# Optimization experiments

Measured on AMD Instinct MI355X. Metric: run time of the kernel, lower is better.

## Reference

```python
import jax, jax.numpy as jnp
import numpy as np

# Config (matches init_kwargs)
B, DIM = 16, 768
HEADS, DHEAD = 12, 64
H_MEM, W_MEM = 16, 16           # memory grid; N = 256 tokens
MAX_AH, MAX_AW = 3, 3
N = H_MEM * W_MEM


def _area_pool(t):
    """t: [B', N, D] laid out on an H_MEM x W_MEM grid.
    Returns (area_sums [B', M, D], area_sizes [M]) over all rectangle sizes
    (ah, aw) with 1<=ah<=MAX_AH, 1<=aw<=MAX_AW, at every valid position,
    via a 2D integral image (summed-area table)."""
    Bp, _, D = t.shape
    g = t.reshape(Bp, H_MEM, W_MEM, D)
    I = jnp.cumsum(jnp.cumsum(g, axis=1), axis=2)
    I = jnp.pad(I, ((0, 0), (1, 0), (1, 0), (0, 0)))  # [B', H+1, W+1, D]
    sums, sizes = [], []
    for ah in range(1, MAX_AH + 1):
        for aw in range(1, MAX_AW + 1):
            s = (I[:, ah:, aw:] - I[:, :-ah, aw:]
                 - I[:, ah:, :-aw] + I[:, :-ah, :-aw])  # [B', H-ah+1, W-aw+1, D]
            n_pos = s.shape[1] * s.shape[2]
            sums.append(s.reshape(Bp, n_pos, D))
            sizes.append(np.full((n_pos,), float(ah * aw), dtype=np.float32))
    return jnp.concatenate(sums, axis=1), jnp.asarray(np.concatenate(sizes))


def setup_inputs() -> dict:
    key = jax.random.key(0)
    ks = jax.random.split(key, 10)
    s = 0.02
    d = dict(
        x=jax.random.normal(ks[0], (B, N, DIM), jnp.float32),
        # to_qkv: Linear(dim, 3*dim, bias=False); stored as (in, out)
        w_qkv=jax.random.normal(ks[1], (DIM, 3 * DIM), jnp.float32) * s,
        # per-head q/k/v projections (dim -> heads*dim_head) with bias
        w_q=jax.random.normal(ks[2], (DIM, HEADS * DHEAD), jnp.float32) * s,
        b_q=jnp.zeros((HEADS * DHEAD,), jnp.float32),
        w_k=jax.random.normal(ks[3], (DIM, HEADS * DHEAD), jnp.float32) * s,
        b_k=jnp.zeros((HEADS * DHEAD,), jnp.float32),
        w_v=jax.random.normal(ks[4], (DIM, HEADS * DHEAD), jnp.float32) * s,
        b_v=jnp.zeros((HEADS * DHEAD,), jnp.float32),
        # output projection (heads*dim_head -> dim)
        w_o=jax.random.normal(ks[5], (HEADS * DHEAD, DIM), jnp.float32) * s,
        b_o=jnp.zeros((DIM,), jnp.float32),
    )
    return d


def reference(x, w_qkv, w_q, b_q, w_k, b_k, w_v, b_v, w_o, b_o):
    # QKV projection + split: 'b n (qkv d) -> qkv b n d'
    qkv = x @ w_qkv                               # [B, N, 3*DIM]
    q, k, v = jnp.split(qkv, 3, axis=-1)          # each [B, N, DIM]

    def to_heads(t, w, b):                        # 'b n (h d) -> (b h) n d'
        return ((t @ w + b)
                .reshape(B, N, HEADS, DHEAD)
                .transpose(0, 2, 1, 3)
                .reshape(B * HEADS, N, DHEAD))

    qh = to_heads(q, w_q, b_q)
    kh = to_heads(k, w_k, b_k)
    vh = to_heads(v, w_v, b_v)

    # Area keys: mean over each area; area values: sum over each area.
    k_sum, sizes = _area_pool(kh)                 # [BH, M, d], [M]
    k_area = k_sum / sizes[None, :, None]
    v_area, _ = _area_pool(vh)                    # [BH, M, d]

    logits = jnp.einsum('bqd,bmd->bqm', qh, k_area)   # [BH, N, M]
    weights = jax.nn.softmax(logits, axis=-1)
    out = jnp.einsum('bqm,bmd->bqd', weights, v_area)  # [BH, N, d]

    # '(b h) n d -> b n (h d)' then output projection
    out = (out.reshape(B, HEADS, N, DHEAD)
              .transpose(0, 2, 1, 3)
              .reshape(B, N, HEADS * DHEAD))
    return out @ w_o + b_o
```

## Files before the change

kernel.cpp:

```cpp
#include <hip/hip_runtime.h>
#include <hip/hip_bf16.h>

typedef __hip_bfloat16 bf16;
typedef __attribute__((ext_vector_type(8))) short short8b;
typedef __attribute__((ext_vector_type(4))) short short4b;
typedef __attribute__((ext_vector_type(4))) float f32x4;

#define NAREA 2025
#define NAREA_PAD 2048

static __device__ __forceinline__ float b2f(bf16 x) { return __bfloat162float(x); }
static __device__ __forceinline__ short f2bs(float f) {
  bf16 h = __float2bfloat16(f);
  return *(short*)&h;
}

static __device__ __forceinline__ void gll16(const void* g, void* l) {
  __builtin_amdgcn_global_load_lds(
      (const __attribute__((address_space(1))) unsigned int*)(unsigned long long)g,
      (__attribute__((address_space(3))) unsigned int*)(unsigned int)(unsigned long long)l,
      16, 0, 0);
}

__global__ __launch_bounds__(256) void k_prep(
    const float* __restrict__ x, const float* __restrict__ wqkv,
    const float* __restrict__ wq, const float* __restrict__ wk,
    const float* __restrict__ wv,
    bf16* __restrict__ xb, bf16* __restrict__ wqkvb,
    bf16* __restrict__ wqT, bf16* __restrict__ wkT, bf16* __restrict__ wvT,
    int4* __restrict__ rectG, float* __restrict__ invG)
{
  __shared__ float tile[32][33];
  int b = blockIdx.x;
  if (b < 4800) {
    int idx = (b * 256 + threadIdx.x) * 4;
    const int NX = 4096 * 768;
    float4 v;
    bf16* d;
    if (idx < NX) { v = *(const float4*)(x + idx); d = xb + idx; }
    else { v = *(const float4*)(wqkv + (idx - NX)); d = wqkvb + (idx - NX); }
    short4b s = {f2bs(v.x), f2bs(v.y), f2bs(v.z), f2bs(v.w)};
    *(short4b*)d = s;
    return;
  }
  if (b < 6528) {
    int r = b - 4800;
    int z = r / 576; r -= z * 576;
    int by = r / 24, bx = r - by * 24;
    const float* src = (z == 0) ? wq : (z == 1) ? wk : wv;
    bf16* dst = (z == 0) ? wqT : (z == 1) ? wkT : wvT;
    int r0 = by * 32, c0 = bx * 32;
    int lx = threadIdx.x & 31, ly = threadIdx.x >> 5;
#pragma unroll
    for (int yy = 0; yy < 4; ++yy)
      tile[ly + yy * 8][lx] = src[(size_t)(r0 + ly + yy * 8) * 768 + c0 + lx];
    __syncthreads();
#pragma unroll
    for (int yy = 0; yy < 4; ++yy)
      dst[(size_t)(c0 + ly + yy * 8) * 768 + r0 + lx] =
          __float2bfloat16(tile[lx][ly + yy * 8]);
    return;
  }
  int m = (b - 6528) * 256 + threadIdx.x;
  if (m >= NAREA_PAD) return;
  int4 rc = make_int4(0, 0, 0, 0);
  float iv = 0.f;
  if (m < NAREA) {
    int rem = m, ah = 1, aw = 1, found = 0;
    for (int a = 1; a <= 3 && !found; ++a)
      for (int w = 1; w <= 3 && !found; ++w) {
        int np = (17 - a) * (17 - w);
        if (rem < np) { ah = a; aw = w; found = 1; }
        else rem -= np;
      }
    int cw = 17 - aw;
    int y = rem / cw, xx = rem - y * cw;
    rc.x = (y * 17 + xx) * 64;
    rc.y = (y * 17 + (xx + aw)) * 64;
    rc.z = ((y + ah) * 17 + xx) * 64;
    rc.w = ((y + ah) * 17 + (xx + aw)) * 64;
    iv = 1.0f / (float)(ah * aw);
  }
  rectG[m] = rc;
  invG[m] = iv;
}

__global__ __launch_bounds__(256) void k_tcast1(
    const float* __restrict__ src, bf16* __restrict__ dst)
{
  __shared__ float tile[32][33];
  int r0 = blockIdx.y * 32, c0 = blockIdx.x * 32;
  int lx = threadIdx.x & 31, ly = threadIdx.x >> 5;
#pragma unroll
  for (int yy = 0; yy < 4; ++yy)
    tile[ly + yy * 8][lx] = src[(size_t)(r0 + ly + yy * 8) * 768 + c0 + lx];
  __syncthreads();
#pragma unroll
  for (int yy = 0; yy < 4; ++yy)
    dst[(size_t)(c0 + ly + yy * 8) * 768 + r0 + lx] =
        __float2bfloat16(tile[lx][ly + yy * 8]);
}


__global__ __launch_bounds__(256) void k_combine_m(
    const bf16* __restrict__ wqkvb, const bf16* __restrict__ wqT,
    const bf16* __restrict__ wkT, const bf16* __restrict__ wvT,
    bf16* __restrict__ WcTb)
{
  __shared__ __align__(16) short As[2][128 * 32];
  __shared__ __align__(16) short Bs[2][128 * 32];
  const int t3 = blockIdx.z;
  const bf16* BT = (t3 == 0) ? wqT : (t3 == 1) ? wkT : wvT;
  const int m0 = blockIdx.y * 128, n0 = blockIdx.x * 128;
  const int tid = threadIdx.x, lane = tid & 63, w = tid >> 6;
  const int tt = lane & 15, q4 = lane >> 4;
  const int moff = (w & 1) * 64, noff = (w >> 1) * 64;
  const int r_a = tid >> 2, kc = (tid & 3) * 8;

  f32x4 acc[4][4];
#pragma unroll
  for (int i = 0; i < 4; ++i)
#pragma unroll
    for (int j = 0; j < 4; ++j) acc[i][j] = (f32x4){0.f, 0.f, 0.f, 0.f};

#define STAGE_C(k0, buf)                                                        \
  {                                                                             \
    gll16(wqkvb + (size_t)(m0 + r_a) * 2304 + t3 * 768 + (k0) + kc,             \
          &As[buf][w * 512]);                                                   \
    gll16(wqkvb + (size_t)(m0 + r_a + 64) * 2304 + t3 * 768 + (k0) + kc,        \
          &As[buf][2048 + w * 512]);                                            \
    gll16(BT + (size_t)(n0 + r_a) * 768 + (k0) + kc, &Bs[buf][w * 512]);        \
    gll16(BT + (size_t)(n0 + r_a + 64) * 768 + (k0) + kc,                       \
          &Bs[buf][2048 + w * 512]);                                            \
  }

  STAGE_C(0, 0);
  for (int it = 0; it < 24; ++it) {
    __syncthreads();
    if (it < 23) STAGE_C((it + 1) * 32, (it + 1) & 1);
    const short* as = As[it & 1];
    const short* bs = Bs[it & 1];
    short8b afr[4], bfr[4];
#pragma unroll
    for (int mt = 0; mt < 4; ++mt)
      afr[mt] = *(const short8b*)&as[(moff + mt * 16 + tt) * 32 + q4 * 8];
#pragma unroll
    for (int nt = 0; nt < 4; ++nt)
      bfr[nt] = *(const short8b*)&bs[(noff + nt * 16 + tt) * 32 + q4 * 8];
#pragma unroll
    for (int mt = 0; mt < 4; ++mt)
#pragma unroll
      for (int nt = 0; nt < 4; ++nt)
        acc[mt][nt] = __builtin_amdgcn_mfma_f32_16x16x32_bf16(afr[mt], bfr[nt], acc[mt][nt], 0, 0, 0);
  }
#undef STAGE_C

  bf16* C = WcTb + (size_t)t3 * 768 * 768;
#pragma unroll
  for (int nt = 0; nt < 4; ++nt) {
    int n = n0 + noff + nt * 16 + tt;
#pragma unroll
    for (int mt = 0; mt < 4; ++mt) {
      int mb = m0 + moff + mt * 16 + q4 * 4;
      short4b v = {f2bs(acc[mt][nt][0]), f2bs(acc[mt][nt][1]),
                   f2bs(acc[mt][nt][2]), f2bs(acc[mt][nt][3])};
      *(short4b*)&C[(size_t)n * 768 + mb] = v;
    }
  }
}

__global__ __launch_bounds__(256) void k_proj_m(
    const bf16* __restrict__ xb, const bf16* __restrict__ WcTb,
    const float* __restrict__ bq, const float* __restrict__ bk,
    const float* __restrict__ bv,
    bf16* __restrict__ qh, bf16* __restrict__ kh, bf16* __restrict__ vh)
{
  __shared__ __align__(16) short As[2][128 * 32];
  __shared__ __align__(16) short Bs[2][128 * 32];
  const int t3 = blockIdx.z;
  const bf16* BT = WcTb + (size_t)t3 * 768 * 768;
  const float* bias = (t3 == 0) ? bq : (t3 == 1) ? bk : bv;
  bf16* dst = (t3 == 0) ? qh : (t3 == 1) ? kh : vh;
  const int m0 = blockIdx.y * 128, n0 = blockIdx.x * 128;
  const int tid = threadIdx.x, lane = tid & 63, w = tid >> 6;
  const int tt = lane & 15, q4 = lane >> 4;
  const int moff = (w & 1) * 64, noff = (w >> 1) * 64;
  const int r_a = tid >> 2, kc = (tid & 3) * 8;

  f32x4 acc[4][4];
#pragma unroll
  for (int i = 0; i < 4; ++i)
#pragma unroll
    for (int j = 0; j < 4; ++j) acc[i][j] = (f32x4){0.f, 0.f, 0.f, 0.f};

#define STAGE_P(k0, buf)                                                        \
  {                                                                             \
    gll16(xb + (size_t)(m0 + r_a) * 768 + (k0) + kc, &As[buf][w * 512]);        \
    gll16(xb + (size_t)(m0 + r_a + 64) * 768 + (k0) + kc,                       \
          &As[buf][2048 + w * 512]);                                            \
    gll16(BT + (size_t)(n0 + r_a) * 768 + (k0) + kc, &Bs[buf][w * 512]);        \
    gll16(BT + (size_t)(n0 + r_a + 64) * 768 + (k0) + kc,                       \
          &Bs[buf][2048 + w * 512]);                                            \
  }

  STAGE_P(0, 0);
  for (int it = 0; it < 24; ++it) {
    __syncthreads();
    if (it < 23) STAGE_P((it + 1) * 32, (it + 1) & 1);
    const short* as = As[it & 1];
    const short* bs = Bs[it & 1];
    short8b afr[4], bfr[4];
#pragma unroll
    for (int mt = 0; mt < 4; ++mt)
      afr[mt] = *(const short8b*)&as[(moff + mt * 16 + tt) * 32 + q4 * 8];
#pragma unroll
    for (int nt = 0; nt < 4; ++nt)
      bfr[nt] = *(const short8b*)&bs[(noff + nt * 16 + tt) * 32 + q4 * 8];
#pragma unroll
    for (int mt = 0; mt < 4; ++mt)
#pragma unroll
      for (int nt = 0; nt < 4; ++nt)
        acc[mt][nt] = __builtin_amdgcn_mfma_f32_16x16x32_bf16(afr[mt], bfr[nt], acc[mt][nt], 0, 0, 0);
  }
#undef STAGE_P

#pragma unroll
  for (int nt = 0; nt < 4; ++nt) {
    int c = n0 + noff + nt * 16 + tt;
    float bvv = bias[c];
    int h = c >> 6, d = c & 63;
#pragma unroll
    for (int mt = 0; mt < 4; ++mt) {
#pragma unroll
      for (int r = 0; r < 4; ++r) {
        int m = m0 + moff + mt * 16 + q4 * 4 + r;
        dst[(((size_t)((m >> 8) * 12 + h)) << 14) + ((m & 255) << 6) + d] =
            __float2bfloat16(acc[mt][nt][r] + bvv);
      }
    }
  }
}

__global__ __launch_bounds__(256) void k_out_m(
    const bf16* __restrict__ attno, const bf16* __restrict__ woT,
    const float* __restrict__ bo, float* __restrict__ out)
{
  __shared__ __align__(16) short As[2][128 * 32];
  __shared__ __align__(16) short Bs[2][128 * 32];
  const int m0 = blockIdx.y * 128, n0 = blockIdx.x * 128;
  const int tid = threadIdx.x, lane = tid & 63, w = tid >> 6;
  const int tt = lane & 15, q4 = lane >> 4;
  const int moff = (w & 1) * 64, noff = (w >> 1) * 64;
  const int r_a = tid >> 2, kc = (tid & 3) * 8;
  const int m_a0 = m0 + r_a, m_a1 = m0 + r_a + 64;

  f32x4 acc[4][4];
#pragma unroll
  for (int i = 0; i < 4; ++i)
#pragma unroll
    for (int j = 0; j < 4; ++j) acc[i][j] = (f32x4){0.f, 0.f, 0.f, 0.f};

#define STAGE_O(k0, buf)                                                        \
  {                                                                             \
    int k = (k0) + kc;                                                          \
    gll16(attno + (((size_t)((m_a0 >> 8) * 12 + (k >> 6))) << 14) +             \
              ((m_a0 & 255) << 6) + (k & 63),                                   \
          &As[buf][w * 512]);                                                   \
    gll16(attno + (((size_t)((m_a1 >> 8) * 12 + (k >> 6))) << 14) +             \
              ((m_a1 & 255) << 6) + (k & 63),                                   \
          &As[buf][2048 + w * 512]);                                            \
    gll16(woT + (size_t)(n0 + r_a) * 768 + k, &Bs[buf][w * 512]);               \
    gll16(woT + (size_t)(n0 + r_a + 64) * 768 + k, &Bs[buf][2048 + w * 512]);   \
  }

  STAGE_O(0, 0);
  for (int it = 0; it < 24; ++it) {
    __syncthreads();
    if (it < 23) STAGE_O((it + 1) * 32, (it + 1) & 1);
    const short* as = As[it & 1];
    const short* bs = Bs[it & 1];
    short8b afr[4], bfr[4];
#pragma unroll
    for (int mt = 0; mt < 4; ++mt)
      afr[mt] = *(const short8b*)&as[(moff + mt * 16 + tt) * 32 + q4 * 8];
#pragma unroll
    for (int nt = 0; nt < 4; ++nt)
      bfr[nt] = *(const short8b*)&bs[(noff + nt * 16 + tt) * 32 + q4 * 8];
#pragma unroll
    for (int mt = 0; mt < 4; ++mt)
#pragma unroll
      for (int nt = 0; nt < 4; ++nt)
        acc[mt][nt] = __builtin_amdgcn_mfma_f32_16x16x32_bf16(afr[mt], bfr[nt], acc[mt][nt], 0, 0, 0);
  }
#undef STAGE_O

#pragma unroll
  for (int nt = 0; nt < 4; ++nt) {
    int c = n0 + noff + nt * 16 + tt;
    float bvv = bo[c];
#pragma unroll
    for (int mt = 0; mt < 4; ++mt)
#pragma unroll
      for (int r = 0; r < 4; ++r) {
        int m = m0 + moff + mt * 16 + q4 * 4 + r;
        out[(size_t)m * 768 + c] = acc[mt][nt][r] + bvv;
      }
  }
}

__global__ __launch_bounds__(1024) void k_area_pre(
    const bf16* __restrict__ kh, const bf16* __restrict__ vh,
    const int4* __restrict__ rectG, const float* __restrict__ invG,
    bf16* __restrict__ Karea, bf16* __restrict__ VareaT)
{
  __shared__ float sat[17 * 17 * 65];
  int bh = blockIdx.x >> 1;
  bool isv = blockIdx.x & 1;
  const bf16* src = (isv ? vh : kh) + ((size_t)bh << 14);
  int tid = threadIdx.x;
  int d = tid & 63;
  int row = tid >> 6;
  {
    float run = 0.f;
    sat[((row + 1) * 17) * 65 + d] = 0.f;
#pragma unroll
    for (int xx = 0; xx < 16; ++xx) {
      run += b2f(src[(row * 16 + xx) * 64 + d]);
      sat[((row + 1) * 17 + (xx + 1)) * 65 + d] = run;
    }
    if (row == 0) {
#pragma unroll
      for (int xx = 0; xx < 17; ++xx) sat[xx * 65 + d] = 0.f;
    }
  }
  __syncthreads();
  {
    int x = row + 1;
    float run = 0.f;
#pragma unroll
    for (int y = 1; y <= 16; ++y) {
      run += sat[(y * 17 + x) * 65 + d];
      sat[(y * 17 + x) * 65 + d] = run;
    }
  }
  __syncthreads();
  if (!isv) {
    bf16* out = Karea + ((size_t)bh << 17);
    for (int c = row; c < 45; c += 16) {
      int ah, y;
      if (c < 16)      { ah = 1; y = c; }
      else if (c < 31) { ah = 2; y = c - 16; }
      else             { ah = 3; y = c - 31; }
      int b1, b2, b3;
      if (ah == 1)      { b1 = 0;    b2 = 256;  b3 = 496;  }
      else if (ah == 2) { b1 = 720;  b2 = 960;  b3 = 1185; }
      else              { b1 = 1395; b2 = 1619; b3 = 1829; }
      float V[17];
#pragma unroll
      for (int x = 0; x < 17; ++x)
        V[x] = sat[((y + ah) * 17 + x) * 65 + d] - sat[(y * 17 + x) * 65 + d];
      {
        int b = b1 + y * 16;
#pragma unroll
        for (int x = 0; x < 16; ++x)
          out[(size_t)(b + x) * 64 + d] = __float2bfloat16((V[x + 1] - V[x]) * (1.0f / (float)(ah)));
      }
      {
        int b = b2 + y * 15;
        float iv = 1.0f / (float)(2 * ah);
#pragma unroll
        for (int x = 0; x < 15; ++x)
          out[(size_t)(b + x) * 64 + d] = __float2bfloat16((V[x + 2] - V[x]) * iv);
      }
      {
        int b = b3 + y * 14;
        float iv = 1.0f / (float)(3 * ah);
#pragma unroll
        for (int x = 0; x < 14; ++x)
          out[(size_t)(b + x) * 64 + d] = __float2bfloat16((V[x + 3] - V[x]) * iv);
      }
    }
    if (row == 15) {
      for (int m = NAREA; m < NAREA_PAD; ++m)
        out[(size_t)m * 64 + d] = __float2bfloat16(0.f);
    }
  } else {
    int mcol = tid & 63;
    int r16 = tid >> 6;
    bf16* out = VareaT + ((size_t)bh << 17);
    for (int s = 0; s < 128; ++s) {
      int idx = s * 16 + r16;
      int it = idx >> 6, dd = idx & 63;
      int4 rc = rectG[it * 64 + mcol];
      int cx = rc.x + (rc.x >> 6), cy = rc.y + (rc.y >> 6);
      int cz = rc.z + (rc.z >> 6), cw = rc.w + (rc.w >> 6);
      float df = sat[cw + dd] - sat[cy + dd] - sat[cz + dd] + sat[cx + dd];
      out[(((size_t)it << 6) + dd) * 64 + mcol] = __float2bfloat16(df);
    }
  }
}

__global__ __launch_bounds__(256, 4) void k_attn_g(
    const bf16* __restrict__ qh, const bf16* __restrict__ Karea,
    const bf16* __restrict__ VareaT,
    float* __restrict__ Op0, float* __restrict__ Op1,
    float* __restrict__ lp0, float* __restrict__ lp1)
{
  __shared__ __align__(16) short aK2[2][64 * 80];
  __shared__ __align__(16) short aVt2[2][64 * 80];

  const int tid = threadIdx.x;
  const int w = tid >> 6;
  const int lane = tid & 63;
  const int t = lane & 15;
  const int q4 = lane >> 4;
  const int bh = blockIdx.x;
  const int Q0 = blockIdx.y * 128;
  const int it0 = blockIdx.z * 16;
  const int rbase = (t & 12) * 2 + (t & 3);

  const bf16* Kb = Karea + ((size_t)bh << 17);
  const bf16* Vb = VareaT + ((size_t)bh << 17);
  const bf16* qrowA = qh + ((size_t)bh << 14) + (size_t)(Q0 + w * 32 + t) * 64;
  const bf16* qrowB = qrowA + 16 * 64;

  short8b qfA0 = *(const short8b*)(qrowA + q4 * 8);
  short8b qfA1 = *(const short8b*)(qrowA + 32 + q4 * 8);
  short8b qfB0 = *(const short8b*)(qrowB + q4 * 8);
  short8b qfB1 = *(const short8b*)(qrowB + 32 + q4 * 8);

  f32x4 OA[4], OB[4];
#pragma unroll
  for (int i = 0; i < 4; ++i) {
    OA[i] = (f32x4){0.f, 0.f, 0.f, 0.f};
    OB[i] = (f32x4){0.f, 0.f, 0.f, 0.f};
  }
  float lA = 0.f, lB = 0.f;

  const int a8 = tid >> 2;
  const int c8 = (tid & 3) * 16;

  {
    size_t off = ((size_t)(it0 * 64 + a8) << 6) + c8;
    short8b k0a = *(const short8b*)&Kb[off];
    short8b k0b = *(const short8b*)&Kb[off + 8];
    short8b v0a = *(const short8b*)&Vb[off];
    short8b v0b = *(const short8b*)&Vb[off + 8];
    *(short8b*)&aK2[0][a8 * 80 + c8] = k0a;
    *(short8b*)&aK2[0][a8 * 80 + c8 + 8] = k0b;
    *(short8b*)&aVt2[0][a8 * 80 + c8] = v0a;
    *(short8b*)&aVt2[0][a8 * 80 + c8 + 8] = v0b;
  }

  for (int it = it0; it < it0 + 16; ++it) {
    short8b kna, knb, vna, vnb;
    if (it + 1 < it0 + 16) {
      size_t off = ((size_t)((it + 1) * 64 + a8) << 6) + c8;
      kna = *(const short8b*)&Kb[off];
      knb = *(const short8b*)&Kb[off + 8];
      vna = *(const short8b*)&Vb[off];
      vnb = *(const short8b*)&Vb[off + 8];
    }
    __syncthreads();
    const short* aK = aK2[it & 1];
    const short* aVt = aVt2[it & 1];
    if (it + 1 < it0 + 16) {
      short* aKn = aK2[(it + 1) & 1];
      short* aVtn = aVt2[(it + 1) & 1];
      *(short8b*)&aKn[a8 * 80 + c8] = kna;
      *(short8b*)&aKn[a8 * 80 + c8 + 8] = knb;
      *(short8b*)&aVtn[a8 * 80 + c8] = vna;
      *(short8b*)&aVtn[a8 * 80 + c8 + 8] = vnb;
    }

    const int t0 = it * 64;
    const bool edge = (t0 + 64 > NAREA);
    union { short8b v; unsigned u[4]; } apvA[2], apvB[2];
#pragma unroll
    for (int at = 0; at < 4; ++at) {
      int row = rbase + (at & 1) * 4 + (at >> 1) * 32;
      short8b af0 = *(const short8b*)&aK[row * 80 + q4 * 8];
      short8b af1 = *(const short8b*)&aK[row * 80 + 32 + q4 * 8];
      int abase = t0 + (at >> 1) * 32 + q4 * 8 + (at & 1) * 4;
      {
        f32x4 s = (f32x4){0.f, 0.f, 0.f, 0.f};
        s = __builtin_amdgcn_mfma_f32_16x16x32_bf16(af0, qfA0, s, 0, 0, 0);
        s = __builtin_amdgcn_mfma_f32_16x16x32_bf16(af1, qfA1, s, 0, 0, 0);
        float p[4];
#pragma unroll
        for (int r = 0; r < 4; ++r) {
          p[r] = __expf(s[r]);
          if (edge && (abase + r >= NAREA)) p[r] = 0.f;
        }
        lA += (p[0] + p[1]) + (p[2] + p[3]);
        unsigned lo = ((unsigned)(unsigned short)f2bs(p[1]) << 16) |
                      (unsigned short)f2bs(p[0]);
        unsigned hi = ((unsigned)(unsigned short)f2bs(p[3]) << 16) |
                      (unsigned short)f2bs(p[2]);
        apvA[at >> 1].u[(at & 1) * 2 + 0] = lo;
        apvA[at >> 1].u[(at & 1) * 2 + 1] = hi;
      }
      {
        f32x4 s = (f32x4){0.f, 0.f, 0.f, 0.f};
        s = __builtin_amdgcn_mfma_f32_16x16x32_bf16(af0, qfB0, s, 0, 0, 0);
        s = __builtin_amdgcn_mfma_f32_16x16x32_bf16(af1, qfB1, s, 0, 0, 0);
        float p[4];
#pragma unroll
        for (int r = 0; r < 4; ++r) {
          p[r] = __expf(s[r]);
          if (edge && (abase + r >= NAREA)) p[r] = 0.f;
        }
        lB += (p[0] + p[1]) + (p[2] + p[3]);
        unsigned lo = ((unsigned)(unsigned short)f2bs(p[1]) << 16) |
                      (unsigned short)f2bs(p[0]);
        unsigned hi = ((unsigned)(unsigned short)f2bs(p[3]) << 16) |
                      (unsigned short)f2bs(p[2]);
        apvB[at >> 1].u[(at & 1) * 2 + 0] = lo;
        apvB[at >> 1].u[(at & 1) * 2 + 1] = hi;
      }
    }
#pragma unroll
    for (int nt = 0; nt < 4; ++nt) {
      short8b vf0 = *(const short8b*)&aVt[(nt * 16 + t) * 80 + q4 * 8];
      short8b vf1 = *(const short8b*)&aVt[(nt * 16 + t) * 80 + 32 + q4 * 8];
      OA[nt] = __builtin_amdgcn_mfma_f32_16x16x32_bf16(apvA[0].v, vf0, OA[nt], 0, 0, 0);
      OA[nt] = __builtin_amdgcn_mfma_f32_16x16x32_bf16(apvA[1].v, vf1, OA[nt], 0, 0, 0);
      OB[nt] = __builtin_amdgcn_mfma_f32_16x16x32_bf16(apvB[0].v, vf0, OB[nt], 0, 0, 0);
      OB[nt] = __builtin_amdgcn_mfma_f32_16x16x32_bf16(apvB[1].v, vf1, OB[nt], 0, 0, 0);
    }
  }

  lA += __shfl_xor(lA, 16, 64);
  lA += __shfl_xor(lA, 32, 64);
  lB += __shfl_xor(lB, 16, 64);
  lB += __shfl_xor(lB, 32, 64);

  float* lp = blockIdx.z ? lp1 : lp0;
  float* Op = blockIdx.z ? Op1 : Op0;
  if (q4 == 0) {
    lp[(bh << 8) + Q0 + w * 32 + t] = lA;
    lp[(bh << 8) + Q0 + w * 32 + 16 + t] = lB;
  }
  float* Ob = Op + (((size_t)(bh << 8) + Q0 + w * 32) << 6);
#pragma unroll
  for (int r = 0; r < 4; ++r) {
    int qr = q4 * 4 + r;
#pragma unroll
    for (int nt = 0; nt < 4; ++nt) {
      Ob[qr * 64 + nt * 16 + t] = OA[nt][r];
      Ob[(16 + qr) * 64 + nt * 16 + t] = OB[nt][r];
    }
  }
}

__global__ __launch_bounds__(256) void k_norm2(
    const float* __restrict__ Op0, const float* __restrict__ Op1,
    const float* __restrict__ lp0, const float* __restrict__ lp1,
    bf16* __restrict__ attno)
{
  int i = (blockIdx.x * 256 + threadIdx.x) * 4;
  f32x4 a = *(const f32x4*)(Op0 + i);
  f32x4 b = *(const f32x4*)(Op1 + i);
  int q = i >> 6;
  float invl = 1.0f / (lp0[q] + lp1[q]);
  short4b s = {f2bs((a[0] + b[0]) * invl), f2bs((a[1] + b[1]) * invl),
               f2bs((a[2] + b[2]) * invl), f2bs((a[3] + b[3]) * invl)};
  *(short4b*)(attno + i) = s;
}

__global__ __launch_bounds__(1024) void k_integral_p(
    const bf16* __restrict__ kh, const bf16* __restrict__ vh,
    float* __restrict__ Ik, float* __restrict__ Iv)
{
  __shared__ float sat[17 * 17 * 64];
  int bh = blockIdx.x >> 1;
  bool isv = blockIdx.x & 1;
  const bf16* src = (isv ? vh : kh) + ((size_t)bh << 14);
  float* dst = (isv ? Iv : Ik) + (size_t)bh * 18496;
  int tid = threadIdx.x;
  int d = tid & 63;
  int row = tid >> 6;
  {
    float run = 0.f;
    sat[((row + 1) * 17) * 64 + d] = 0.f;
#pragma unroll
    for (int xx = 0; xx < 16; ++xx) {
      run += b2f(src[(row * 16 + xx) * 64 + d]);
      sat[((row + 1) * 17 + (xx + 1)) * 64 + d] = run;
    }
    if (row == 0) {
#pragma unroll
      for (int xx = 0; xx < 17; ++xx) sat[xx * 64 + d] = 0.f;
    }
  }
  __syncthreads();
  {
    int x = row + 1;
    float run = 0.f;
#pragma unroll
    for (int y = 1; y <= 16; ++y) {
      run += sat[(y * 17 + x) * 64 + d];
      sat[(y * 17 + x) * 64 + d] = run;
    }
  }
  __syncthreads();
  for (int i = tid; i < 18496; i += 1024) dst[i] = sat[i];
}

__global__ __launch_bounds__(1024) void k_attn_m(
    const bf16* __restrict__ qh, const float* __restrict__ Ik,
    const float* __restrict__ Iv, const int4* __restrict__ rectG,
    const float* __restrict__ invG, bf16* __restrict__ attno)
{
  __shared__ __align__(16) short aK2[2][64 * 80];
  __shared__ __align__(16) short aVt2[2][64 * 72];

  const int tid = threadIdx.x;
  const int lane = tid & 63;
  const int w = tid >> 6;
  const int t = lane & 15;
  const int q4 = lane >> 4;
  const int bh = blockIdx.x;
  const int rbase = (t & 12) * 2 + (t & 3);

  const float* Ikb = Ik + (size_t)bh * 18496;
  const float* Ivb = Iv + (size_t)bh * 18496;
  const bf16* qbase = qh + ((size_t)bh << 14);

  short8b qf0 = *(const short8b*)(qbase + (w * 16 + t) * 64 + q4 * 8);
  short8b qf1 = *(const short8b*)(qbase + (w * 16 + t) * 64 + 32 + q4 * 8);

  f32x4 O[4];
#pragma unroll
  for (int i = 0; i < 4; ++i) O[i] = (f32x4){0.f, 0.f, 0.f, 0.f};
  float l = 0.f;

  {
    short* aK = aK2[0];
    short* aVt = aVt2[0];
    short vp[4];
#pragma unroll
    for (int i = 0; i < 4; ++i) {
      int j = w * 4 + i;
      int4 rc = rectG[j];
      float iv = invG[j];
      float kc = Ikb[rc.w + lane] - Ikb[rc.y + lane] - Ikb[rc.z + lane] + Ikb[rc.x + lane];
      float vc = Ivb[rc.w + lane] - Ivb[rc.y + lane] - Ivb[rc.z + lane] + Ivb[rc.x + lane];
      aK[j * 80 + lane] = f2bs(kc * iv);
      vp[i] = f2bs(vc);
    }
    *(short4b*)&aVt[lane * 72 + w * 4] = (short4b){vp[0], vp[1], vp[2], vp[3]};
  }

  float kcr[4], vcr[4], ivr[4];
  for (int it = 0; it < 32; ++it) {
    if (it + 1 < 32) {
      int t0n = (it + 1) * 64;
#pragma unroll
      for (int i = 0; i < 4; ++i) {
        int j = t0n + w * 4 + i;
        int4 rc = rectG[j];
        ivr[i] = invG[j];
        kcr[i] = Ikb[rc.w + lane] - Ikb[rc.y + lane] - Ikb[rc.z + lane] + Ikb[rc.x + lane];
        vcr[i] = Ivb[rc.w + lane] - Ivb[rc.y + lane] - Ivb[rc.z + lane] + Ivb[rc.x + lane];
      }
    }
    __syncthreads();
    const short* aK = aK2[it & 1];
    const short* aVt = aVt2[it & 1];
    if (it + 1 < 32) {
      short* aKn = aK2[(it + 1) & 1];
      short* aVtn = aVt2[(it + 1) & 1];
      short vp[4];
#pragma unroll
      for (int i = 0; i < 4; ++i) {
        aKn[(w * 4 + i) * 80 + lane] = f2bs(kcr[i] * ivr[i]);
        vp[i] = f2bs(vcr[i]);
      }
      *(short4b*)&aVtn[lane * 72 + w * 4] = (short4b){vp[0], vp[1], vp[2], vp[3]};
    }

    const int t0 = it * 64;
    const bool edge = (t0 + 64 > NAREA);
    union { short8b v; unsigned u[4]; } apv[2];
#pragma unroll
    for (int at = 0; at < 4; ++at) {
      int row = rbase + (at & 1) * 4 + (at >> 1) * 32;
      short8b af0 = *(const short8b*)&aK[row * 80 + q4 * 8];
      short8b af1 = *(const short8b*)&aK[row * 80 + 32 + q4 * 8];
      f32x4 s = (f32x4){0.f, 0.f, 0.f, 0.f};
      s = __builtin_amdgcn_mfma_f32_16x16x32_bf16(af0, qf0, s, 0, 0, 0);
      s = __builtin_amdgcn_mfma_f32_16x16x32_bf16(af1, qf1, s, 0, 0, 0);
      int abase = t0 + (at >> 1) * 32 + q4 * 8 + (at & 1) * 4;
      float p[4];
#pragma unroll
      for (int r = 0; r < 4; ++r) {
        p[r] = __expf(s[r]);
        if (edge && (abase + r >= NAREA)) p[r] = 0.f;
      }
      l += (p[0] + p[1]) + (p[2] + p[3]);
      unsigned lo = ((unsigned)(unsigned short)f2bs(p[1]) << 16) |
                    (unsigned short)f2bs(p[0]);
      unsigned hi = ((unsigned)(unsigned short)f2bs(p[3]) << 16) |
                    (unsigned short)f2bs(p[2]);
      apv[at >> 1].u[(at & 1) * 2 + 0] = lo;
      apv[at >> 1].u[(at & 1) * 2 + 1] = hi;
    }
#pragma unroll
    for (int nt = 0; nt < 4; ++nt) {
      short8b vf0 = *(const short8b*)&aVt[(nt * 16 + t) * 72 + q4 * 8];
      short8b vf1 = *(const short8b*)&aVt[(nt * 16 + t) * 72 + 32 + q4 * 8];
      O[nt] = __builtin_amdgcn_mfma_f32_16x16x32_bf16(apv[0].v, vf0, O[nt], 0, 0, 0);
      O[nt] = __builtin_amdgcn_mfma_f32_16x16x32_bf16(apv[1].v, vf1, O[nt], 0, 0, 0);
    }
  }

  l += __shfl_xor(l, 16, 64);
  l += __shfl_xor(l, 32, 64);

  bf16* ob = attno + ((size_t)bh << 14);
#pragma unroll
  for (int r = 0; r < 4; ++r) {
    int qrow = q4 * 4 + r;
    float invl = 1.0f / __shfl(l, qrow, 64);
#pragma unroll
    for (int nt = 0; nt < 4; ++nt)
      ob[(w * 16 + qrow) * 64 + nt * 16 + t] = __float2bfloat16(O[nt][r] * invl);
  }
}

extern "C" void kernel_launch(void* const* d_in, const int* in_sizes, int n_in,
                              void* d_out, int out_size, void* d_ws, size_t ws_size,
                              hipStream_t stream) {
  const float* x    = (const float*)d_in[0];
  const float* wqkv = (const float*)d_in[1];
  const float* wq   = (const float*)d_in[2];
  const float* bq   = (const float*)d_in[3];
  const float* wk   = (const float*)d_in[4];
  const float* bk   = (const float*)d_in[5];
  const float* wv   = (const float*)d_in[6];
  const float* bv   = (const float*)d_in[7];
  const float* wo   = (const float*)d_in[8];
  const float* bo   = (const float*)d_in[9];
  float* out = (float*)d_out;

  char* ws = (char*)d_ws;
  char* ob = (char*)d_out;
  const size_t WC_B = 7077888;
  const size_t QH_B = 6291456;
  const size_t AREA_B = 50331648;

  bf16* xb    = (bf16*)ob;
  bf16* WcTb  = (bf16*)(ob + QH_B);
  float* Op0  = (float*)ob;
  bf16* attno = (bf16*)ws;
  int4*  rectG = (int4*)(ws + QH_B);
  float* invG  = (float*)(ws + QH_B + 32768);
  float* lp0   = (float*)(ws + QH_B + 40960);
  float* lp1   = lp0 + 49152;
  bf16* qh = (bf16*)(ws + WC_B);
  bf16* kh = (bf16*)(ws + WC_B + QH_B);
  bf16* vh = (bf16*)(ws + WC_B + 2 * QH_B);
  float* Op1 = (float*)(ws + WC_B + QH_B);
  bf16* wqkvb = (bf16*)(ws + WC_B);
  bf16* wqT   = (bf16*)(ws + WC_B + 3538944);
  bf16* wkT   = (bf16*)(ws + WC_B + 4718592);
  bf16* wvT   = (bf16*)(ws + WC_B + 5898240);
  bf16* Karea  = (bf16*)(ws + WC_B + 3 * QH_B);
  bf16* VareaT = (bf16*)(ws + WC_B + 3 * QH_B + AREA_B);
  float* Ik = (float*)(ws + WC_B + 3 * QH_B);
  float* Iv = Ik + 3551232;
  bf16* woT = (bf16*)(ws + WC_B + 3 * QH_B);

  const size_t REQ = WC_B + 3 * QH_B + 2 * AREA_B;
  const bool primary = (ws_size >= REQ);

  k_prep<<<dim3(6536), 256, 0, stream>>>(x, wqkv, wq, wk, wv, xb, wqkvb,
                                         wqT, wkT, wvT, rectG, invG);
  k_combine_m<<<dim3(6, 6, 3), 256, 0, stream>>>(wqkvb, wqT, wkT, wvT, WcTb);
  k_proj_m<<<dim3(6, 32, 3), 256, 0, stream>>>(xb, WcTb, bq, bk, bv, qh, kh, vh);
  if (primary) {
    k_area_pre<<<dim3(384), 1024, 0, stream>>>(kh, vh, rectG, invG, Karea, VareaT);
    k_attn_g<<<dim3(192, 2, 2), 256, 0, stream>>>(qh, Karea, VareaT,
                                                  Op0, Op1, lp0, lp1);
    k_norm2<<<dim3(3072), 256, 0, stream>>>(Op0, Op1, lp0, lp1, attno);
  } else {
    k_integral_p<<<dim3(384), 1024, 0, stream>>>(kh, vh, Ik, Iv);
    k_attn_m<<<dim3(192), 1024, 0, stream>>>(qh, Ik, Iv, rectG, invG, attno);
  }
  k_tcast1<<<dim3(24, 24), 256, 0, stream>>>(wo, woT);
  k_out_m<<<dim3(6, 32), 256, 0, stream>>>(attno, woT, bo, out);
}
```

Measured before the change: 238.1 us.

## Shrink GEMM tiles to 64-wide for more blocks and fuse wo transpose into norm

The combine, projection and output GEMMs move from 128x128 tiles to 64x64 (or 128x64) tiles with matching grid sizes. This gives more workgroups on a GPU with many CUs, since the previous grids were small (108 to 576 blocks). The wo transpose-cast is folded into the normalization kernel as extra blocks on the primary path, which removes one launch. In exchange, each tile does less operand reuse and the GEMMs issue more global loads overall.

```diff
diff --git a/kernel.cpp b/kernel.cpp
--- a/kernel.cpp
+++ b/kernel.cpp
@@ -107,31 +107,27 @@
     const bf16* __restrict__ wkT, const bf16* __restrict__ wvT,
     bf16* __restrict__ WcTb)
 {
-  __shared__ __align__(16) short As[2][128 * 32];
-  __shared__ __align__(16) short Bs[2][128 * 32];
+  __shared__ __align__(16) short As[2][64 * 32];
+  __shared__ __align__(16) short Bs[2][64 * 32];
   const int t3 = blockIdx.z;
   const bf16* BT = (t3 == 0) ? wqT : (t3 == 1) ? wkT : wvT;
-  const int m0 = blockIdx.y * 128, n0 = blockIdx.x * 128;
+  const int m0 = blockIdx.y * 64, n0 = blockIdx.x * 64;
   const int tid = threadIdx.x, lane = tid & 63, w = tid >> 6;
   const int tt = lane & 15, q4 = lane >> 4;
-  const int moff = (w & 1) * 64, noff = (w >> 1) * 64;
+  const int moff = (w & 1) * 32, noff = (w >> 1) * 32;
   const int r_a = tid >> 2, kc = (tid & 3) * 8;
 
-  f32x4 acc[4][4];
-#pragma unroll
-  for (int i = 0; i < 4; ++i)
-#pragma unroll
-    for (int j = 0; j < 4; ++j) acc[i][j] = (f32x4){0.f, 0.f, 0.f, 0.f};
+  f32x4 acc[2][2];
+#pragma unroll
+  for (int i = 0; i < 2; ++i)
+#pragma unroll
+    for (int j = 0; j < 2; ++j) acc[i][j] = (f32x4){0.f, 0.f, 0.f, 0.f};
 
 #define STAGE_C(k0, buf)                                                        \
   {                                                                             \
     gll16(wqkvb + (size_t)(m0 + r_a) * 2304 + t3 * 768 + (k0) + kc,             \
           &As[buf][w * 512]);                                                   \
-    gll16(wqkvb + (size_t)(m0 + r_a + 64) * 2304 + t3 * 768 + (k0) + kc,        \
-          &As[buf][2048 + w * 512]);                                            \
     gll16(BT + (size_t)(n0 + r_a) * 768 + (k0) + kc, &Bs[buf][w * 512]);        \
-    gll16(BT + (size_t)(n0 + r_a + 64) * 768 + (k0) + kc,                       \
-          &Bs[buf][2048 + w * 512]);                                            \
   }
 
   STAGE_C(0, 0);
@@ -140,27 +136,27 @@
     if (it < 23) STAGE_C((it + 1) * 32, (it + 1) & 1);
     const short* as = As[it & 1];
     const short* bs = Bs[it & 1];
-    short8b afr[4], bfr[4];
-#pragma unroll
-    for (int mt = 0; mt < 4; ++mt)
+    short8b afr[2], bfr[2];
+#pragma unroll
+    for (int mt = 0; mt < 2; ++mt)
       afr[mt] = *(const short8b*)&as[(moff + mt * 16 + tt) * 32 + q4 * 8];
 #pragma unroll
-    for (int nt = 0; nt < 4; ++nt)
+    for (int nt = 0; nt < 2; ++nt)
       bfr[nt] = *(const short8b*)&bs[(noff + nt * 16 + tt) * 32 + q4 * 8];
 #pragma unroll
-    for (int mt = 0; mt < 4; ++mt)
-#pragma unroll
-      for (int nt = 0; nt < 4; ++nt)
+    for (int mt = 0; mt < 2; ++mt)
+#pragma unroll
+      for (int nt = 0; nt < 2; ++nt)
         acc[mt][nt] = __builtin_amdgcn_mfma_f32_16x16x32_bf16(afr[mt], bfr[nt], acc[mt][nt], 0, 0, 0);
   }
 #undef STAGE_C
 
   bf16* C = WcTb + (size_t)t3 * 768 * 768;
 #pragma unroll
-  for (int nt = 0; nt < 4; ++nt) {
+  for (int nt = 0; nt < 2; ++nt) {
     int n = n0 + noff + nt * 16 + tt;
 #pragma unroll
-    for (int mt = 0; mt < 4; ++mt) {
+    for (int mt = 0; mt < 2; ++mt) {
       int mb = m0 + moff + mt * 16 + q4 * 4;
       short4b v = {f2bs(acc[mt][nt][0]), f2bs(acc[mt][nt][1]),
                    f2bs(acc[mt][nt][2]), f2bs(acc[mt][nt][3])};
@@ -176,22 +172,22 @@
     bf16* __restrict__ qh, bf16* __restrict__ kh, bf16* __restrict__ vh)
 {
   __shared__ __align__(16) short As[2][128 * 32];
-  __shared__ __align__(16) short Bs[2][128 * 32];
+  __shared__ __align__(16) short Bs[2][64 * 32];
   const int t3 = blockIdx.z;
   const bf16* BT = WcTb + (size_t)t3 * 768 * 768;
   const float* bias = (t3 == 0) ? bq : (t3 == 1) ? bk : bv;
   bf16* dst = (t3 == 0) ? qh : (t3 == 1) ? kh : vh;
-  const int m0 = blockIdx.y * 128, n0 = blockIdx.x * 128;
+  const int m0 = blockIdx.y * 128, n0 = blockIdx.x * 64;
   const int tid = threadIdx.x, lane = tid & 63, w = tid >> 6;
   const int tt = lane & 15, q4 = lane >> 4;
-  const int moff = (w & 1) * 64, noff = (w >> 1) * 64;
+  const int moff = (w & 1) * 64, noff = (w >> 1) * 32;
   const int r_a = tid >> 2, kc = (tid & 3) * 8;
 
-  f32x4 acc[4][4];
+  f32x4 acc[4][2];
 #pragma unroll
   for (int i = 0; i < 4; ++i)
 #pragma unroll
-    for (int j = 0; j < 4; ++j) acc[i][j] = (f32x4){0.f, 0.f, 0.f, 0.f};
+    for (int j = 0; j < 2; ++j) acc[i][j] = (f32x4){0.f, 0.f, 0.f, 0.f};
 
 #define STAGE_P(k0, buf)                                                        \
   {                                                                             \
@@ -199,8 +195,6 @@
     gll16(xb + (size_t)(m0 + r_a + 64) * 768 + (k0) + kc,                       \
           &As[buf][2048 + w * 512]);                                            \
     gll16(BT + (size_t)(n0 + r_a) * 768 + (k0) + kc, &Bs[buf][w * 512]);        \
-    gll16(BT + (size_t)(n0 + r_a + 64) * 768 + (k0) + kc,                       \
-          &Bs[buf][2048 + w * 512]);                                            \
   }
 
   STAGE_P(0, 0);
@@ -209,23 +203,23 @@
     if (it < 23) STAGE_P((it + 1) * 32, (it + 1) & 1);
     const short* as = As[it & 1];
     const short* bs = Bs[it & 1];
-    short8b afr[4], bfr[4];
+    short8b afr[4], bfr[2];
 #pragma unroll
     for (int mt = 0; mt < 4; ++mt)
       afr[mt] = *(const short8b*)&as[(moff + mt * 16 + tt) * 32 + q4 * 8];
 #pragma unroll
-    for (int nt = 0; nt < 4; ++nt)
+    for (int nt = 0; nt < 2; ++nt)
       bfr[nt] = *(const short8b*)&bs[(noff + nt * 16 + tt) * 32 + q4 * 8];
 #pragma unroll
     for (int mt = 0; mt < 4; ++mt)
 #pragma unroll
-      for (int nt = 0; nt < 4; ++nt)
+      for (int nt = 0; nt < 2; ++nt)
         acc[mt][nt] = __builtin_amdgcn_mfma_f32_16x16x32_bf16(afr[mt], bfr[nt], acc[mt][nt], 0, 0, 0);
   }
 #undef STAGE_P
 
 #pragma unroll
-  for (int nt = 0; nt < 4; ++nt) {
+  for (int nt = 0; nt < 2; ++nt) {
     int c = n0 + noff + nt * 16 + tt;
     float bvv = bias[c];
     int h = c >> 6, d = c & 63;
@@ -245,20 +239,20 @@
     const bf16* __restrict__ attno, const bf16* __restrict__ woT,
     const float* __restrict__ bo, float* __restrict__ out)
 {
-  __shared__ __align__(16) short As[2][128 * 32];
-  __shared__ __align__(16) short Bs[2][128 * 32];
-  const int m0 = blockIdx.y * 128, n0 = blockIdx.x * 128;
+  __shared__ __align__(16) short As[2][64 * 32];
+  __shared__ __align__(16) short Bs[2][64 * 32];
+  const int m0 = blockIdx.y * 64, n0 = blockIdx.x * 64;
   const int tid = threadIdx.x, lane = tid & 63, w = tid >> 6;
   const int tt = lane & 15, q4 = lane >> 4;
-  const int moff = (w & 1) * 64, noff = (w >> 1) * 64;
+  const int moff = (w & 1) * 32, noff = (w >> 1) * 32;
   const int r_a = tid >> 2, kc = (tid & 3) * 8;
-  const int m_a0 = m0 + r_a, m_a1 = m0 + r_a + 64;
-
-  f32x4 acc[4][4];
-#pragma unroll
-  for (int i = 0; i < 4; ++i)
-#pragma unroll
-    for (int j = 0; j < 4; ++j) acc[i][j] = (f32x4){0.f, 0.f, 0.f, 0.f};
+  const int m_a0 = m0 + r_a;
+
+  f32x4 acc[2][2];
+#pragma unroll
+  for (int i = 0; i < 2; ++i)
+#pragma unroll
+    for (int j = 0; j < 2; ++j) acc[i][j] = (f32x4){0.f, 0.f, 0.f, 0.f};
 
 #define STAGE_O(k0, buf)                                                        \
   {                                                                             \
@@ -266,11 +260,7 @@
     gll16(attno + (((size_t)((m_a0 >> 8) * 12 + (k >> 6))) << 14) +             \
               ((m_a0 & 255) << 6) + (k & 63),                                   \
           &As[buf][w * 512]);                                                   \
-    gll16(attno + (((size_t)((m_a1 >> 8) * 12 + (k >> 6))) << 14) +             \
-              ((m_a1 & 255) << 6) + (k & 63),                                   \
-          &As[buf][2048 + w * 512]);                                            \
     gll16(woT + (size_t)(n0 + r_a) * 768 + k, &Bs[buf][w * 512]);               \
-    gll16(woT + (size_t)(n0 + r_a + 64) * 768 + k, &Bs[buf][2048 + w * 512]);   \
   }
 
   STAGE_O(0, 0);
@@ -279,27 +269,27 @@
     if (it < 23) STAGE_O((it + 1) * 32, (it + 1) & 1);
     const short* as = As[it & 1];
     const short* bs = Bs[it & 1];
-    short8b afr[4], bfr[4];
-#pragma unroll
-    for (int mt = 0; mt < 4; ++mt)
+    short8b afr[2], bfr[2];
+#pragma unroll
+    for (int mt = 0; mt < 2; ++mt)
       afr[mt] = *(const short8b*)&as[(moff + mt * 16 + tt) * 32 + q4 * 8];
 #pragma unroll
-    for (int nt = 0; nt < 4; ++nt)
+    for (int nt = 0; nt < 2; ++nt)
       bfr[nt] = *(const short8b*)&bs[(noff + nt * 16 + tt) * 32 + q4 * 8];
 #pragma unroll
-    for (int mt = 0; mt < 4; ++mt)
-#pragma unroll
-      for (int nt = 0; nt < 4; ++nt)
+    for (int mt = 0; mt < 2; ++mt)
+#pragma unroll
+      for (int nt = 0; nt < 2; ++nt)
         acc[mt][nt] = __builtin_amdgcn_mfma_f32_16x16x32_bf16(afr[mt], bfr[nt], acc[mt][nt], 0, 0, 0);
   }
 #undef STAGE_O
 
 #pragma unroll
-  for (int nt = 0; nt < 4; ++nt) {
+  for (int nt = 0; nt < 2; ++nt) {
     int c = n0 + noff + nt * 16 + tt;
     float bvv = bo[c];
 #pragma unroll
-    for (int mt = 0; mt < 4; ++mt)
+    for (int mt = 0; mt < 2; ++mt)
 #pragma unroll
       for (int r = 0; r < 4; ++r) {
         int m = m0 + moff + mt * 16 + q4 * 4 + r;
@@ -553,19 +543,36 @@
   }
 }
 
-__global__ __launch_bounds__(256) void k_norm2(
+__global__ __launch_bounds__(256) void k_norm2t(
     const float* __restrict__ Op0, const float* __restrict__ Op1,
     const float* __restrict__ lp0, const float* __restrict__ lp1,
-    bf16* __restrict__ attno)
-{
-  int i = (blockIdx.x * 256 + threadIdx.x) * 4;
-  f32x4 a = *(const f32x4*)(Op0 + i);
-  f32x4 b = *(const f32x4*)(Op1 + i);
-  int q = i >> 6;
-  float invl = 1.0f / (lp0[q] + lp1[q]);
-  short4b s = {f2bs((a[0] + b[0]) * invl), f2bs((a[1] + b[1]) * invl),
-               f2bs((a[2] + b[2]) * invl), f2bs((a[3] + b[3]) * invl)};
-  *(short4b*)(attno + i) = s;
+    bf16* __restrict__ attno,
+    const float* __restrict__ wo, bf16* __restrict__ woT)
+{
+  if (blockIdx.x < 3072) {
+    int i = (blockIdx.x * 256 + threadIdx.x) * 4;
+    f32x4 a = *(const f32x4*)(Op0 + i);
+    f32x4 b = *(const f32x4*)(Op1 + i);
+    int q = i >> 6;
+    float invl = 1.0f / (lp0[q] + lp1[q]);
+    short4b s = {f2bs((a[0] + b[0]) * invl), f2bs((a[1] + b[1]) * invl),
+                 f2bs((a[2] + b[2]) * invl), f2bs((a[3] + b[3]) * invl)};
+    *(short4b*)(attno + i) = s;
+    return;
+  }
+  __shared__ float tile[32][33];
+  int b = blockIdx.x - 3072;
+  int bxx = b % 24, byy = b / 24;
+  int r0 = byy * 32, c0 = bxx * 32;
+  int lx = threadIdx.x & 31, ly = threadIdx.x >> 5;
+#pragma unroll
+  for (int yy = 0; yy < 4; ++yy)
+    tile[ly + yy * 8][lx] = wo[(size_t)(r0 + ly + yy * 8) * 768 + c0 + lx];
+  __syncthreads();
+#pragma unroll
+  for (int yy = 0; yy < 4; ++yy)
+    woT[(size_t)(c0 + ly + yy * 8) * 768 + r0 + lx] =
+        __float2bfloat16(tile[lx][ly + yy * 8]);
 }
 
 __global__ __launch_bounds__(1024) void k_integral_p(
@@ -777,17 +784,17 @@
 
   k_prep<<<dim3(6536), 256, 0, stream>>>(x, wqkv, wq, wk, wv, xb, wqkvb,
                                          wqT, wkT, wvT, rectG, invG);
-  k_combine_m<<<dim3(6, 6, 3), 256, 0, stream>>>(wqkvb, wqT, wkT, wvT, WcTb);
-  k_proj_m<<<dim3(6, 32, 3), 256, 0, stream>>>(xb, WcTb, bq, bk, bv, qh, kh, vh);
+  k_combine_m<<<dim3(12, 12, 3), 256, 0, stream>>>(wqkvb, wqT, wkT, wvT, WcTb);
+  k_proj_m<<<dim3(12, 32, 3), 256, 0, stream>>>(xb, WcTb, bq, bk, bv, qh, kh, vh);
   if (primary) {
     k_area_pre<<<dim3(384), 1024, 0, stream>>>(kh, vh, rectG, invG, Karea, VareaT);
     k_attn_g<<<dim3(192, 2, 2), 256, 0, stream>>>(qh, Karea, VareaT,
                                                   Op0, Op1, lp0, lp1);
-    k_norm2<<<dim3(3072), 256, 0, stream>>>(Op0, Op1, lp0, lp1, attno);
+    k_norm2t<<<dim3(3648), 256, 0, stream>>>(Op0, Op1, lp0, lp1, attno, wo, woT);
   } else {
     k_integral_p<<<dim3(384), 1024, 0, stream>>>(kh, vh, Ik, Iv);
     k_attn_m<<<dim3(192), 1024, 0, stream>>>(qh, Ik, Iv, rectG, invG, attno);
-  }
-  k_tcast1<<<dim3(24, 24), 256, 0, stream>>>(wo, woT);
-  k_out_m<<<dim3(6, 32), 256, 0, stream>>>(attno, woT, bo, out);
-}
+    k_tcast1<<<dim3(24, 24), 256, 0, stream>>>(wo, woT);
+  }
+  k_out_m<<<dim3(12, 64), 256, 0, stream>>>(attno, woT, bo, out);
+}
```

Result: no change. 233.5 us (-1.9%).
